# Optimization experiments

Hardware: AMD Instinct MI355X
Metric: run time of the kernel (lower is better)

Reference implementation:

```python
import jax, jax.numpy as jnp
import numpy as np
from jax import lax

WINDOW_SIZE = 11
SIGMA = 1.5
CHANNEL = 1
C1 = 0.01 ** 2
C2 = 0.03 ** 2
EPS = 1e-8


def _gaussian_window(window_size, sigma, channel):
    coords = jnp.arange(window_size, dtype=jnp.float32) - window_size // 2
    g = jnp.exp(-coords ** 2 / (2.0 * sigma ** 2))
    g = g / g.sum()
    w2d = jnp.outer(g, g)  # [ws, ws]
    # depthwise conv kernel, OIHW with I=1 (groups=channel)
    return jnp.broadcast_to(w2d[None, None], (channel, 1, window_size, window_size))


def _blur(x, window, channel):
    # depthwise 2D conv, SAME padding (padding = ws//2 for odd ws)
    return lax.conv_general_dilated(
        x, window, window_strides=(1, 1), padding="SAME",
        feature_group_count=channel,
        dimension_numbers=("NCHW", "OIHW", "NCHW"))


def setup_inputs() -> dict:
    key = jax.random.key(0)
    k1, k2 = jax.random.split(key)
    B, C, H, W = 32, CHANNEL, 512, 512
    pred = jax.random.uniform(k1, (B, C, H, W), dtype=jnp.float32)
    target = jax.random.uniform(k2, (B, C, H, W), dtype=jnp.float32)
    window = _gaussian_window(WINDOW_SIZE, SIGMA, CHANNEL)
    return {"pred": pred, "target": target, "window": window}


def reference(pred, target, window):
    channel = pred.shape[1]
    mu_p = _blur(pred, window, channel)
    mu_t = _blur(target, window, channel)
    mu_p_sq = mu_p ** 2
    mu_t_sq = mu_t ** 2
    mu_pt = mu_p * mu_t
    sigma_p_sq = _blur(pred ** 2, window, channel) - mu_p_sq
    sigma_t_sq = _blur(target ** 2, window, channel) - mu_t_sq
    sigma_pt = _blur(pred * target, window, channel) - mu_pt
    sigma_p_sq = jnp.maximum(sigma_p_sq, 0.0)
    sigma_t_sq = jnp.maximum(sigma_t_sq, 0.0)
    numerator = (2.0 * mu_pt + C1) * (2.0 * sigma_pt + C2)
    denominator = (mu_p_sq + mu_t_sq + C1) * (sigma_p_sq + sigma_t_sq + C2)
    ssim_map = numerator / (denominator + EPS)
    return 1.0 - jnp.mean(ssim_map)
```

## Files before the change

kernel.cpp:

```cpp
#include <hip/hip_runtime.h>

typedef _Float16 f16x2 __attribute__((ext_vector_type(2)));
typedef _Float16 f16x4 __attribute__((ext_vector_type(4)));
typedef _Float16 f16x8 __attribute__((ext_vector_type(8)));
typedef float    f32x4 __attribute__((ext_vector_type(4)));

#define NBLK 4096

__device__ __forceinline__ f16x2 pkrtz(float a, float b) {
    return __builtin_bit_cast(f16x2, __builtin_amdgcn_cvt_pkrtz(a, b));
}

__global__ __launch_bounds__(256, 3)
void ssim_fused(const float* __restrict__ pred,
                const float* __restrict__ targ,
                const float* __restrict__ win,
                float* __restrict__ partial)
{
    __shared__ __align__(16) _Float16 rawT[2 * 80 * 64];
    __shared__ __align__(16) _Float16 vbuf[4 * 32 * 88];
    __shared__ float gw[16];
    __shared__ float wsum[4];

    const int tid  = threadIdx.x;
    const int lane = tid & 63;
    const int wv   = tid >> 6;
    const int bid  = blockIdx.x;
    const int b    = bid >> 7;
    const int rem  = bid & 127;
    const int ty   = rem >> 3;
    const int tx   = rem & 7;
    const int x0g  = tx * 64 - 8;
    const int y0g  = ty * 32 - 8;

    if (tid < 11) {
        float s = 0.f;
        #pragma unroll
        for (int j = 0; j < 11; ++j) s += win[tid * 11 + j];
        gw[tid] = s;
    }

    const float* pb = pred + (size_t)b * (512 * 512);
    const float* tb = targ + (size_t)b * (512 * 512);
    const bool interior = (tx >= 1) & (tx <= 6) & (ty >= 1) & (ty <= 14);

    if (tid < 240) {
        const int xi = tid % 20;
        const int qy = tid / 20;
        const int lx = xi * 4;
        const int gx = x0g + lx;
        const int gy = y0g + qy * 4;
        float4 pr[4], tr[4];
        if (interior) {
            const float* pp = pb + (size_t)gy * 512 + gx;
            const float* tp = tb + (size_t)gy * 512 + gx;
            #pragma unroll
            for (int r = 0; r < 4; ++r) {
                pr[r] = *(const float4*)(pp + r * 512);
                tr[r] = *(const float4*)(tp + r * 512);
            }
        } else {
            const bool xin = (gx >= 0) & (gx + 3 < 512);
            #pragma unroll
            for (int r = 0; r < 4; ++r) {
                const int gyr = gy + r;
                const bool yok = (unsigned)gyr < 512u;
                if (yok && xin) {
                    pr[r] = *(const float4*)(pb + (size_t)gyr * 512 + gx);
                    tr[r] = *(const float4*)(tb + (size_t)gyr * 512 + gx);
                } else {
                    float4 pz = {0.f, 0.f, 0.f, 0.f};
                    float4 tz = {0.f, 0.f, 0.f, 0.f};
                    if (yok) {
                        #pragma unroll
                        for (int e = 0; e < 4; ++e) {
                            const int gxe = gx + e;
                            if ((unsigned)gxe < 512u) {
                                pz[e] = pb[(size_t)gyr * 512 + gxe];
                                tz[e] = tb[(size_t)gyr * 512 + gxe];
                            }
                        }
                    }
                    pr[r] = pz; tr[r] = tz;
                }
            }
        }
        #pragma unroll
        for (int e = 0; e < 4; ++e) {
            const int x  = lx + e;
            const int sw = (x >> 1) & 7;
            const int sc = (qy & 8) | ((qy & 7) ^ sw);
            _Float16* col = &rawT[x * 64 + sc * 4];
            union { f16x2 h2[2]; f16x4 v; } u;
            u.h2[0] = pkrtz(pr[0][e], pr[1][e]);
            u.h2[1] = pkrtz(pr[2][e], pr[3][e]);
            *(f16x4*)col = u.v;
            u.h2[0] = pkrtz(tr[0][e], tr[1][e]);
            u.h2[1] = pkrtz(tr[2][e], tr[3][e]);
            *(f16x4*)(col + 5120) = u.v;
        }
    }
    __syncthreads();

    const int mrow = lane & 15;
    const int quad = lane >> 4;
    f16x8 afr;
    #pragma unroll
    for (int j = 0; j < 8; ++j) {
        const int d = quad * 8 + j - mrow - 3;
        afr[j] = (d >= 0 && d < 11) ? (_Float16)gw[d] : (_Float16)0.f;
    }
    const f32x4 z4 = {0.f, 0.f, 0.f, 0.f};
    const int swr = mrow >> 1;

    #pragma unroll
    for (int c = 0; c < 5; ++c) {
        const int x = c * 16 + mrow;
        const _Float16* bp = &rawT[x * 64];
        #pragma unroll
        for (int h = 0; h < 2; ++h) {
            const int sc0 = h * 4 + 2 * quad;
            const int sc1 = sc0 + 1;
            const int o0  = (((sc0 & 8) | ((sc0 & 7) ^ swr))) << 2;
            const int o1  = (((sc1 & 8) | ((sc1 & 7) ^ swr))) << 2;
            union { f16x4 q[2]; f16x8 v; } pu, tu;
            if (wv != 1) {
                pu.q[0] = *(const f16x4*)&bp[o0];
                pu.q[1] = *(const f16x4*)&bp[o1];
            }
            if (wv != 0) {
                tu.q[0] = *(const f16x4*)&bp[5120 + o0];
                tu.q[1] = *(const f16x4*)&bp[5120 + o1];
            }
            f16x8 frag;
            if      (wv == 0) frag = pu.v;
            else if (wv == 1) frag = tu.v;
            else if (wv == 2) frag = pu.v * pu.v + tu.v * tu.v;
            else              frag = pu.v * tu.v;
            const f32x4 dv = __builtin_amdgcn_mfma_f32_16x16x32_f16(afr, frag, z4, 0, 0, 0);
            _Float16* vb = &vbuf[wv * 2816 + (h * 16 + quad * 4) * 88 + x];
            #pragma unroll
            for (int r = 0; r < 4; ++r)
                vb[r * 88] = (_Float16)dv[r];
        }
    }
    __syncthreads();

    float lsum = 0.f;
    {
        const int X0 = wv * 16;
        #pragma unroll
        for (int yh = 0; yh < 2; ++yh) {
            f32x4 dq[4];
            #pragma unroll
            for (int pl = 0; pl < 4; ++pl) {
                const f16x8 bv = *(const f16x8*)
                    &vbuf[pl * 2816 + (yh * 16 + mrow) * 88 + X0 + quad * 8];
                dq[pl] = __builtin_amdgcn_mfma_f32_16x16x32_f16(afr, bv, z4, 0, 0, 0);
            }
            #pragma unroll
            for (int r = 0; r < 4; ++r) {
                const float mp = dq[0][r], mt = dq[1][r];
                const float sv = dq[2][r], qv = dq[3][r];
                const float mp2 = mp * mp, mt2 = mt * mt, mpt = mp * mt;
                const float sig = fmaxf(sv - mp2 - mt2, 0.f);
                const float cv  = qv - mpt;
                const float num = (2.f * mpt + 1e-4f) * (2.f * cv + 9e-4f);
                const float den = (mp2 + mt2 + 1e-4f) * (sig + 9e-4f);
                lsum += num * __builtin_amdgcn_rcpf(den + 1e-8f);
            }
        }
    }

    #pragma unroll
    for (int off = 32; off > 0; off >>= 1)
        lsum += __shfl_down(lsum, off, 64);
    if (lane == 0) wsum[wv] = lsum;
    __syncthreads();
    if (tid == 0)
        partial[bid] = wsum[0] + wsum[1] + wsum[2] + wsum[3];
}

__global__ __launch_bounds__(256)
void ssim_reduce(const float* __restrict__ partial, float* __restrict__ out)
{
    __shared__ double ws[4];
    double s = 0.0;
    const f32x4* p4 = (const f32x4*)partial;
    for (int i = threadIdx.x; i < NBLK / 4; i += 256) {
        const f32x4 v = p4[i];
        s += (double)v[0] + (double)v[1] + (double)v[2] + (double)v[3];
    }
    #pragma unroll
    for (int off = 32; off > 0; off >>= 1)
        s += __shfl_down(s, off, 64);
    if ((threadIdx.x & 63) == 0) ws[threadIdx.x >> 6] = s;
    __syncthreads();
    if (threadIdx.x == 0) {
        const double tot = ws[0] + ws[1] + ws[2] + ws[3];
        out[0] = (float)(1.0 - tot / 8388608.0);
    }
}

extern "C" void kernel_launch(void* const* d_in, const int* in_sizes, int n_in,
                              void* d_out, int out_size, void* d_ws, size_t ws_size,
                              hipStream_t stream)
{
    const float* pred = (const float*)d_in[0];
    const float* targ = (const float*)d_in[1];
    const float* win  = (const float*)d_in[2];
    float* out     = (float*)d_out;
    float* partial = (float*)d_ws;

    ssim_fused<<<NBLK, 256, 0, stream>>>(pred, targ, win, partial);
    ssim_reduce<<<1, 256, 0, stream>>>(partial, out);
}
```

Before: 120.1 us.

## Halve SSIM tile height, transpose vertical MFMA, vectorize intermediate stores

```diff
diff --git a/kernel.cpp b/kernel.cpp
--- a/kernel.cpp
+++ b/kernel.cpp
@@ -5,20 +5,20 @@
 typedef _Float16 f16x8 __attribute__((ext_vector_type(8)));
 typedef float    f32x4 __attribute__((ext_vector_type(4)));
 
-#define NBLK 4096
+#define NBLK 8192
 
 __device__ __forceinline__ f16x2 pkrtz(float a, float b) {
     return __builtin_bit_cast(f16x2, __builtin_amdgcn_cvt_pkrtz(a, b));
 }
 
-__global__ __launch_bounds__(256, 3)
+__global__ __launch_bounds__(256, 7)
 void ssim_fused(const float* __restrict__ pred,
                 const float* __restrict__ targ,
                 const float* __restrict__ win,
                 float* __restrict__ partial)
 {
-    __shared__ __align__(16) _Float16 rawT[2 * 80 * 64];
-    __shared__ __align__(16) _Float16 vbuf[4 * 32 * 88];
+    __shared__ __align__(16) _Float16 rawT[2 * 80 * 32];
+    __shared__ __align__(16) _Float16 vbuf[4 * 16 * 88];
     __shared__ float gw[16];
     __shared__ float wsum[4];
 
@@ -26,12 +26,12 @@
     const int lane = tid & 63;
     const int wv   = tid >> 6;
     const int bid  = blockIdx.x;
-    const int b    = bid >> 7;
-    const int rem  = bid & 127;
+    const int b    = bid >> 8;
+    const int rem  = bid & 255;
     const int ty   = rem >> 3;
     const int tx   = rem & 7;
     const int x0g  = tx * 64 - 8;
-    const int y0g  = ty * 32 - 8;
+    const int y0g  = ty * 16 - 8;
 
     if (tid < 11) {
         float s = 0.f;
@@ -42,9 +42,9 @@
 
     const float* pb = pred + (size_t)b * (512 * 512);
     const float* tb = targ + (size_t)b * (512 * 512);
-    const bool interior = (tx >= 1) & (tx <= 6) & (ty >= 1) & (ty <= 14);
+    const bool interior = (tx >= 1) & (tx <= 6) & (ty >= 1) & (ty <= 30);
 
-    if (tid < 240) {
+    if (tid < 160) {
         const int xi = tid % 20;
         const int qy = tid / 20;
         const int lx = xi * 4;
@@ -60,44 +60,31 @@
                 tr[r] = *(const float4*)(tp + r * 512);
             }
         } else {
-            const bool xin = (gx >= 0) & (gx + 3 < 512);
+            const bool xin = ((unsigned)gx <= 508u);
             #pragma unroll
             for (int r = 0; r < 4; ++r) {
                 const int gyr = gy + r;
-                const bool yok = (unsigned)gyr < 512u;
-                if (yok && xin) {
+                if (xin && (unsigned)gyr < 512u) {
                     pr[r] = *(const float4*)(pb + (size_t)gyr * 512 + gx);
                     tr[r] = *(const float4*)(tb + (size_t)gyr * 512 + gx);
                 } else {
-                    float4 pz = {0.f, 0.f, 0.f, 0.f};
-                    float4 tz = {0.f, 0.f, 0.f, 0.f};
-                    if (yok) {
-                        #pragma unroll
-                        for (int e = 0; e < 4; ++e) {
-                            const int gxe = gx + e;
-                            if ((unsigned)gxe < 512u) {
-                                pz[e] = pb[(size_t)gyr * 512 + gxe];
-                                tz[e] = tb[(size_t)gyr * 512 + gxe];
-                            }
-                        }
-                    }
-                    pr[r] = pz; tr[r] = tz;
+                    pr[r] = float4{0.f, 0.f, 0.f, 0.f};
+                    tr[r] = float4{0.f, 0.f, 0.f, 0.f};
                 }
             }
         }
         #pragma unroll
         for (int e = 0; e < 4; ++e) {
             const int x  = lx + e;
-            const int sw = (x >> 1) & 7;
-            const int sc = (qy & 8) | ((qy & 7) ^ sw);
-            _Float16* col = &rawT[x * 64 + sc * 4];
+            const int f  = ((x >> 1) ^ (x >> 4)) & 7;
+            _Float16* col = &rawT[x * 32 + ((qy ^ f) << 2)];
             union { f16x2 h2[2]; f16x4 v; } u;
             u.h2[0] = pkrtz(pr[0][e], pr[1][e]);
             u.h2[1] = pkrtz(pr[2][e], pr[3][e]);
             *(f16x4*)col = u.v;
             u.h2[0] = pkrtz(tr[0][e], tr[1][e]);
             u.h2[1] = pkrtz(tr[2][e], tr[3][e]);
-            *(f16x4*)(col + 5120) = u.v;
+            *(f16x4*)(col + 2560) = u.v;
         }
     }
     __syncthreads();
@@ -111,64 +98,55 @@
         afr[j] = (d >= 0 && d < 11) ? (_Float16)gw[d] : (_Float16)0.f;
     }
     const f32x4 z4 = {0.f, 0.f, 0.f, 0.f};
-    const int swr = mrow >> 1;
 
     #pragma unroll
     for (int c = 0; c < 5; ++c) {
         const int x = c * 16 + mrow;
-        const _Float16* bp = &rawT[x * 64];
-        #pragma unroll
-        for (int h = 0; h < 2; ++h) {
-            const int sc0 = h * 4 + 2 * quad;
-            const int sc1 = sc0 + 1;
-            const int o0  = (((sc0 & 8) | ((sc0 & 7) ^ swr))) << 2;
-            const int o1  = (((sc1 & 8) | ((sc1 & 7) ^ swr))) << 2;
-            union { f16x4 q[2]; f16x8 v; } pu, tu;
-            if (wv != 1) {
-                pu.q[0] = *(const f16x4*)&bp[o0];
-                pu.q[1] = *(const f16x4*)&bp[o1];
-            }
-            if (wv != 0) {
-                tu.q[0] = *(const f16x4*)&bp[5120 + o0];
-                tu.q[1] = *(const f16x4*)&bp[5120 + o1];
-            }
-            f16x8 frag;
-            if      (wv == 0) frag = pu.v;
-            else if (wv == 1) frag = tu.v;
-            else if (wv == 2) frag = pu.v * pu.v + tu.v * tu.v;
-            else              frag = pu.v * tu.v;
-            const f32x4 dv = __builtin_amdgcn_mfma_f32_16x16x32_f16(afr, frag, z4, 0, 0, 0);
-            _Float16* vb = &vbuf[wv * 2816 + (h * 16 + quad * 4) * 88 + x];
-            #pragma unroll
-            for (int r = 0; r < 4; ++r)
-                vb[r * 88] = (_Float16)dv[r];
+        const int f = ((x >> 1) ^ (x >> 4)) & 7;
+        const _Float16* bp = &rawT[x * 32];
+        const int o0 = ((2 * quad    ) ^ f) << 2;
+        const int o1 = ((2 * quad + 1) ^ f) << 2;
+        union { f16x4 q[2]; f16x8 v; } pu, tu;
+        if (wv != 1) {
+            pu.q[0] = *(const f16x4*)&bp[o0];
+            pu.q[1] = *(const f16x4*)&bp[o1];
         }
+        if (wv != 0) {
+            tu.q[0] = *(const f16x4*)&bp[2560 + o0];
+            tu.q[1] = *(const f16x4*)&bp[2560 + o1];
+        }
+        f16x8 frag;
+        if      (wv == 0) frag = pu.v;
+        else if (wv == 1) frag = tu.v;
+        else if (wv == 2) frag = pu.v * pu.v + tu.v * tu.v;
+        else              frag = pu.v * tu.v;
+        const f32x4 dv = __builtin_amdgcn_mfma_f32_16x16x32_f16(frag, afr, z4, 0, 0, 0);
+        union { f16x2 h2[2]; f16x4 v; } o;
+        o.h2[0] = pkrtz(dv[0], dv[1]);
+        o.h2[1] = pkrtz(dv[2], dv[3]);
+        *(f16x4*)&vbuf[wv * 1408 + mrow * 88 + c * 16 + quad * 4] = o.v;
     }
     __syncthreads();
 
     float lsum = 0.f;
     {
         const int X0 = wv * 16;
+        f32x4 dq[4];
         #pragma unroll
-        for (int yh = 0; yh < 2; ++yh) {
-            f32x4 dq[4];
-            #pragma unroll
-            for (int pl = 0; pl < 4; ++pl) {
-                const f16x8 bv = *(const f16x8*)
-                    &vbuf[pl * 2816 + (yh * 16 + mrow) * 88 + X0 + quad * 8];
-                dq[pl] = __builtin_amdgcn_mfma_f32_16x16x32_f16(afr, bv, z4, 0, 0, 0);
-            }
-            #pragma unroll
-            for (int r = 0; r < 4; ++r) {
-                const float mp = dq[0][r], mt = dq[1][r];
-                const float sv = dq[2][r], qv = dq[3][r];
-                const float mp2 = mp * mp, mt2 = mt * mt, mpt = mp * mt;
-                const float sig = fmaxf(sv - mp2 - mt2, 0.f);
-                const float cv  = qv - mpt;
-                const float num = (2.f * mpt + 1e-4f) * (2.f * cv + 9e-4f);
-                const float den = (mp2 + mt2 + 1e-4f) * (sig + 9e-4f);
-                lsum += num * __builtin_amdgcn_rcpf(den + 1e-8f);
-            }
+        for (int pl = 0; pl < 4; ++pl) {
+            const f16x8 bv = *(const f16x8*)&vbuf[pl * 1408 + mrow * 88 + X0 + quad * 8];
+            dq[pl] = __builtin_amdgcn_mfma_f32_16x16x32_f16(afr, bv, z4, 0, 0, 0);
+        }
+        #pragma unroll
+        for (int r = 0; r < 4; ++r) {
+            const float mp = dq[0][r], mt = dq[1][r];
+            const float sv = dq[2][r], qv = dq[3][r];
+            const float mp2 = mp * mp, mt2 = mt * mt, mpt = mp * mt;
+            const float sig = fmaxf(sv - mp2 - mt2, 0.f);
+            const float cv  = qv - mpt;
+            const float num = (2.f * mpt + 1e-4f) * (2.f * cv + 9e-4f);
+            const float den = (mp2 + mt2 + 1e-4f) * (sig + 9e-4f);
+            lsum += num * __builtin_amdgcn_rcpf(den + 1e-8f);
         }
     }
 
```

After: 108.5 us. -9.7%, faster.
